# Optimization experiments

Measured on AMD Instinct MI355X. Metric: run time of the kernel, lower is better.

## Reference

```python
import jax, jax.numpy as jnp
import numpy as np

NC = 80
NA = 3
NO = NC + 5  # 85
ANCHORS = jnp.array([[[10.,13.],[16.,30.],[33.,23.]],
                     [[30.,61.],[62.,45.],[59.,119.]],
                     [[116.,90.],[156.,198.],[373.,326.]]], dtype=jnp.float32)
STRIDES = (8.0, 16.0, 32.0)
CONF_THRES = 0.25
IOU_THRES = 0.45
NMS_TOPK = 1000   # fixed candidate count for jit-friendly NMS (YOLO caps at max_nms)
MAX_DET = 300
MAX_WH = 4096.0   # class-offset trick from non_max_suppression


def _decode(x, w, b, anchors, stride):
    # x: [B,C,ny,nx]; w: [255,C]; 1x1 conv == channel matmul
    B, _, ny, nx = x.shape
    y = jnp.einsum('bchw,oc->bohw', x, w) + b[None, :, None, None]
    y = y.reshape(B, NA, NO, ny, nx).transpose(0, 1, 3, 4, 2)  # [B,na,ny,nx,no]
    s = jax.nn.sigmoid(y)
    yv, xv = jnp.meshgrid(jnp.arange(ny, dtype=y.dtype), jnp.arange(nx, dtype=y.dtype), indexing='ij')
    grid = jnp.stack((xv, yv), -1) - 0.5                      # [ny,nx,2]
    xy = (s[..., :2] * 2.0 + grid[None, None]) * stride
    wh = (s[..., 2:4] * 2.0) ** 2 * (anchors * stride)[None, :, None, None, :]
    out = jnp.concatenate((xy, wh, s[..., 4:]), axis=-1)
    return out.reshape(B, NA * ny * nx, NO)


def _xywh2xyxy(x):
    xy, wh = x[..., :2], x[..., 2:4]
    return jnp.concatenate([xy - wh * 0.5, xy + wh * 0.5], axis=-1)


def _box_iou(a, b):
    lt = jnp.maximum(a[:, None, :2], b[None, :, :2])
    rb = jnp.minimum(a[:, None, 2:], b[None, :, 2:])
    wh = jnp.clip(rb - lt, 0.0)
    inter = wh[..., 0] * wh[..., 1]
    area_a = (a[:, 2] - a[:, 0]) * (a[:, 3] - a[:, 1])
    area_b = (b[:, 2] - b[:, 0]) * (b[:, 3] - b[:, 1])
    return inter / (area_a[:, None] + area_b[None, :] - inter + 1e-7)


def _nms_single(pred):
    # pred: [N, 85] -> dets [MAX_DET, 6] = (x1,y1,x2,y2,conf,cls), zero-padded
    boxes = _xywh2xyxy(pred[:, :4])
    obj = pred[:, 4]
    cls_conf = pred[:, 5:] * obj[:, None]          # class scores
    score = jnp.max(cls_conf, axis=-1)
    cls = jnp.argmax(cls_conf, axis=-1)
    score = jnp.where(score > CONF_THRES, score, 0.0)
    top_s, idx = jax.lax.top_k(score, NMS_TOPK)    # fixed candidate set
    b = boxes[idx]                                  # [K,4]
    c = cls[idx].astype(b.dtype)
    bo = b + (c * MAX_WH)[:, None]                  # class-aware offset
    iou = _box_iou(bo, bo)                          # [K,K]
    keep0 = top_s > CONF_THRES
    rng = jnp.arange(NMS_TOPK)

    def body(i, keep):
        sup = (iou[i] > IOU_THRES) & (rng > i)
        return jnp.where(keep[i], keep & (~sup), keep)

    keep = jax.lax.fori_loop(0, NMS_TOPK, body, keep0)
    final_s = jnp.where(keep, top_s, 0.0)
    fs, fi = jax.lax.top_k(final_s, MAX_DET)
    det = jnp.concatenate([b[fi], fs[:, None], c[fi][:, None]], axis=-1)  # [MAX_DET,6]
    det = jnp.where((fs > CONF_THRES)[:, None], det, 0.0)
    return det


def setup_inputs() -> dict:
    key = jax.random.key(0)
    ks = jax.random.split(key, 9)
    B = 16
    return {
        'x0': jax.random.normal(ks[0], (B, 128, 80, 80), jnp.float32),
        'x1': jax.random.normal(ks[1], (B, 256, 40, 40), jnp.float32),
        'x2': jax.random.normal(ks[2], (B, 512, 20, 20), jnp.float32),
        'w0': jax.random.normal(ks[3], (255, 128), jnp.float32) * 0.02,
        'b0': jax.random.normal(ks[4], (255,), jnp.float32) * 0.02,
        'w1': jax.random.normal(ks[5], (255, 256), jnp.float32) * 0.02,
        'b1': jax.random.normal(ks[6], (255,), jnp.float32) * 0.02,
        'w2': jax.random.normal(ks[7], (255, 512), jnp.float32) * 0.02,
        'b2': jax.random.normal(ks[8], (255,), jnp.float32) * 0.02,
    }


def reference(x0, x1, x2, w0, b0, w1, b1, w2, b2):
    z0 = _decode(x0, w0, b0, ANCHORS[0], STRIDES[0])
    z1 = _decode(x1, w1, b1, ANCHORS[1], STRIDES[1])
    z2 = _decode(x2, w2, b2, ANCHORS[2], STRIDES[2])
    pred = jnp.concatenate([z0, z1, z2], axis=1)   # [B, 25200, 85]
    dets = jax.vmap(_nms_single)(pred)             # [B, 300, 6]
    return dets, pred
```

## Files before the change

### kernel.cpp

```cpp
#include <hip/hip_runtime.h>
#include <cstdint>

#define BATCH   16
#define NCLS    80
#define NOUT    85
#define NANC    3
#define NCAND   25200
#define CONF    0.25f
#define IOUT    0.45f
#define TOPK    1000
#define MAXDET  300
#define MAXWH   4096.0f
#define CAPK    2048
#define NBH     520
#define XPAD    40

typedef __attribute__((ext_vector_type(8))) short short8;
typedef __attribute__((ext_vector_type(4))) float f32x4;
typedef unsigned int u32;

constexpr size_t SCORE_OFF = 0;
constexpr size_t CLS_OFF   = SCORE_OFF + (size_t)BATCH * NCAND * 4;
constexpr size_t THR_OFF   = CLS_OFF   + (size_t)BATCH * NCAND * 4;
constexpr size_t CNT_OFF   = THR_OFF   + 256;
constexpr size_t KEYS_OFF  = CNT_OFF   + 256;
constexpr size_t RS_OFF    = KEYS_OFF  + (size_t)BATCH * CAPK * 8;
constexpr size_t RBOX_OFF  = RS_OFF    + (size_t)BATCH * TOPK * 4;
constexpr size_t RBO_OFF   = RBOX_OFF  + (size_t)BATCH * TOPK * 16;
constexpr size_t RCLS_OFF  = RBO_OFF   + (size_t)BATCH * TOPK * 16;
constexpr size_t SUP_OFF   = RCLS_OFF  + (size_t)BATCH * TOPK * 4;
constexpr size_t ORDER_OFF = SUP_OFF   + (size_t)BATCH * TOPK * 16 * 8;
constexpr size_t KC_OFF    = ORDER_OFF + (size_t)BATCH * MAXDET * 4;
constexpr int NL0 = 255 * 128, NL1 = 255 * 256, NL2 = 255 * 512;
constexpr int WB0 = 0, WB1 = 3 * NL0, WB2 = 3 * NL0 + 3 * NL1;

__device__ __forceinline__ ushort bf16rn(float f) {
    uint32_t u = __float_as_uint(f);
    uint32_t r = u + 0x7FFFu + ((u >> 16) & 1u);
    return (ushort)(r >> 16);
}

__device__ __forceinline__ void split3(float v, ushort& s1, ushort& s2, ushort& s3) {
    ushort h1 = bf16rn(v);
    float f1 = __uint_as_float((uint32_t)h1 << 16);
    float r1 = v - f1;
    ushort h2 = bf16rn(r1);
    float f2 = __uint_as_float((uint32_t)h2 << 16);
    ushort h3 = bf16rn(r1 - f2);
    s1 = h1; s2 = h2; s3 = h3;
}

__device__ __forceinline__ void gl_lds16(const float* g, void* l) {
    __builtin_amdgcn_global_load_lds(
        (const __attribute__((address_space(1))) u32*)g,
        (__attribute__((address_space(3))) u32*)l, 16, 0, 0);
}

__global__ __launch_bounds__(256)
void wsplit_kernel(const float* __restrict__ w0, const float* __restrict__ w1,
                   const float* __restrict__ w2, ushort* __restrict__ wsp) {
    int i = blockIdx.x * 256 + threadIdx.x;
    if (i >= NL0 + NL1 + NL2) return;
    const float* src; int idx, base, NL;
    if (i < NL0)            { src = w0; idx = i;             base = WB0; NL = NL0; }
    else if (i < NL0 + NL1) { src = w1; idx = i - NL0;       base = WB1; NL = NL1; }
    else                    { src = w2; idx = i - NL0 - NL1; base = WB2; NL = NL2; }
    ushort s1, s2, s3;
    split3(src[idx], s1, s2, s3);
    wsp[base + idx]          = s1;
    wsp[base + NL + idx]     = s2;
    wsp[base + 2 * NL + idx] = s3;
}

template<int C, int NN>
__device__ __forceinline__ void decode_level(
    const float* __restrict__ xb,
    const ushort* __restrict__ w1p, const ushort* __restrict__ w2p,
    const ushort* __restrict__ w3p, const float* __restrict__ bias,
    float* __restrict__ predB, float* __restrict__ scoreB, int* __restrict__ clsB,
    int tile, int lvlOff, float stride,
    float aw0, float ah0, float aw1, float ah1, float aw2, float ah2,
    char* xsb0, char* xsb1, ushort* x1, ushort* x2, ushort* x3, float* staged)
{
    constexpr int NPOS = NN * NN;
    constexpr int NCHUNK = C / 32;
    constexpr int MAXOFF = C * NPOS - 4;
    const int tid  = threadIdx.x;
    const int lane = tid & 63;
    const int wid  = tid >> 6;
    const int l16  = lane >> 4;
    const int lr   = lane & 15;
    const int pos0 = tile * 64;

    f32x4 acc[4][4];
#pragma unroll
    for (int nf = 0; nf < 4; nf++)
#pragma unroll
        for (int pf = 0; pf < 4; pf++) acc[nf][pf] = (f32x4){0.f, 0.f, 0.f, 0.f};

    const int sp = tid & 63;
    const int wv = tid >> 6;

    char* xsb[2] = {xsb0, xsb1};

#pragma unroll
    for (int i = 0; i < 2; i++) {
        int f = tid + i * 256;
        int kc = f >> 4;
        int p4 = (f & 15) * 4;
        int off = kc * NPOS + pos0 + p4;
        off = off < MAXOFF ? off : MAXOFF;
        gl_lds16(xb + off, xsb[0] + f * 16);
    }

    for (int c = 0; c < NCHUNK; c++) {
        float* xs = (float*)xsb[c & 1];
        __syncthreads();
        if (c + 1 < NCHUNK) {
            const int k0n = (c + 1) * 32;
#pragma unroll
            for (int i = 0; i < 2; i++) {
                int f = tid + i * 256;
                int kc = f >> 4;
                int p4 = (f & 15) * 4;
                int off = (k0n + kc) * NPOS + pos0 + p4;
                off = off < MAXOFF ? off : MAXOFF;
                gl_lds16(xb + off, xsb[(c + 1) & 1] + f * 16);
            }
        }
        {
            short8 s1v, s2v, s3v;
#pragma unroll
            for (int j = 0; j < 8; j++) {
                float f = xs[(wv * 8 + j) * 64 + sp];
                ushort u1, u2, u3;
                split3(f, u1, u2, u3);
                s1v[j] = (short)u1; s2v[j] = (short)u2; s3v[j] = (short)u3;
            }
            int dst = sp * XPAD + ((wv ^ ((sp >> 2) & 3)) << 3);
            *(short8*)(x1 + dst) = s1v;
            *(short8*)(x2 + dst) = s2v;
            *(short8*)(x3 + dst) = s3v;
        }
        asm volatile("s_waitcnt lgkmcnt(0)" ::: "memory");
        __builtin_amdgcn_s_barrier();
        __builtin_amdgcn_sched_barrier(0);
        short8 b1[4], b2[4], b3[4];
#pragma unroll
        for (int pf = 0; pf < 4; pf++) {
            int pr = pf * 16 + lr;
            int off = pr * XPAD + ((l16 ^ (lr >> 2)) << 3);
            b1[pf] = *(const short8*)(x1 + off);
            b2[pf] = *(const short8*)(x2 + off);
            b3[pf] = *(const short8*)(x3 + off);
        }
        const int k0 = c * 32;
#pragma unroll
        for (int nf = 0; nf < 4; nf++) {
            int o = wid * 64 + nf * 16 + lr;
            int oc = o < 255 ? o : 254;
            size_t aoff = (size_t)oc * C + k0 + l16 * 8;
            short8 A1 = *(const short8*)(w1p + aoff);
            short8 A2 = *(const short8*)(w2p + aoff);
            short8 A3 = *(const short8*)(w3p + aoff);
#pragma unroll
            for (int pf = 0; pf < 4; pf++) {
                acc[nf][pf] = __builtin_amdgcn_mfma_f32_16x16x32_bf16(A1, b1[pf], acc[nf][pf], 0, 0, 0);
                acc[nf][pf] = __builtin_amdgcn_mfma_f32_16x16x32_bf16(A1, b2[pf], acc[nf][pf], 0, 0, 0);
                acc[nf][pf] = __builtin_amdgcn_mfma_f32_16x16x32_bf16(A2, b1[pf], acc[nf][pf], 0, 0, 0);
                acc[nf][pf] = __builtin_amdgcn_mfma_f32_16x16x32_bf16(A2, b2[pf], acc[nf][pf], 0, 0, 0);
                acc[nf][pf] = __builtin_amdgcn_mfma_f32_16x16x32_bf16(A1, b3[pf], acc[nf][pf], 0, 0, 0);
                acc[nf][pf] = __builtin_amdgcn_mfma_f32_16x16x32_bf16(A3, b1[pf], acc[nf][pf], 0, 0, 0);
            }
        }
    }

    float bv[16];
#pragma unroll
    for (int nf = 0; nf < 4; nf++)
#pragma unroll
        for (int r = 0; r < 4; r++) {
            int o = wid * 64 + nf * 16 + l16 * 4 + r;
            bv[nf * 4 + r] = (o < 255) ? bias[o] : 0.f;
        }

    const float aw[3] = {aw0, aw1, aw2};
    const float ah[3] = {ah0, ah1, ah2};
    const int validP = (NPOS - pos0) < 64 ? (NPOS - pos0) : 64;

#pragma unroll
    for (int a = 0; a < 3; a++) {
        __syncthreads();
#pragma unroll
        for (int nf = 0; nf < 4; nf++) {
#pragma unroll
            for (int r = 0; r < 4; r++) {
                int o = wid * 64 + nf * 16 + l16 * 4 + r;
                int j = o - a * 85;
                if (o < 255 && j >= 0 && j < 85) {
#pragma unroll
                    for (int pf = 0; pf < 4; pf++) {
                        int p = pf * 16 + lr;
                        int pos = pos0 + p;
                        float y = acc[nf][pf][r] + bv[nf * 4 + r];
                        float s = 1.f / (1.f + __expf(-y));
                        float val;
                        if (j == 0) {
                            int gyi = pos / NN;
                            float gx = (float)(pos - gyi * NN);
                            val = (2.f * s + gx - 0.5f) * stride;
                        } else if (j == 1) {
                            float gy = (float)(pos / NN);
                            val = (2.f * s + gy - 0.5f) * stride;
                        } else if (j == 2) {
                            float t2 = 2.f * s; val = t2 * t2 * aw[a];
                        } else if (j == 3) {
                            float t2 = 2.f * s; val = t2 * t2 * ah[a];
                        } else {
                            val = s;
                        }
                        staged[p * 85 + j] = val;
                    }
                }
            }
        }
        __syncthreads();
        size_t base = ((size_t)lvlOff + (size_t)a * NPOS + pos0) * 85;
        int tot = validP * 85;
        for (int q = tid; q < tot; q += 256)
            predB[base + q] = staged[q];
        int p = tid >> 2, c4 = tid & 3;
        if (p < validP) {
            int j0 = 5 + c4 * 20;
            float best = staged[p * 85 + j0];
            int bi = c4 * 20;
#pragma unroll
            for (int jj = 1; jj < 20; jj++) {
                float vv = staged[p * 85 + j0 + jj];
                if (vv > best) { best = vv; bi = c4 * 20 + jj; }
            }
#pragma unroll
            for (int d = 1; d < 4; d <<= 1) {
                float ov = __shfl_xor(best, d);
                int   oi = __shfl_xor(bi, d);
                if (ov > best || (ov == best && oi < bi)) { best = ov; bi = oi; }
            }
            if (c4 == 0) {
                float obj = staged[p * 85 + 4];
                float sc = obj * best;
                int cand = lvlOff + a * NPOS + pos0 + p;
                scoreB[cand] = (sc > CONF) ? sc : 0.f;
                clsB[cand] = bi;
            }
        }
    }
}

__global__ __launch_bounds__(256)
void decode_all_kernel(const float* __restrict__ x0, const float* __restrict__ x1,
                       const float* __restrict__ x2,
                       const float* __restrict__ b0, const float* __restrict__ b1,
                       const float* __restrict__ b2,
                       const ushort* __restrict__ wsp,
                       float* __restrict__ pred,
                       float* __restrict__ scoreArr, int* __restrict__ clsArr)
{
    __shared__ __align__(16) char smem[31744];
    char*   xsb0 = smem;
    char*   xsb1 = smem + 8192;
    ushort* p1   = (ushort*)(smem + 16384);
    ushort* p2   = (ushort*)(smem + 21504);
    ushort* p3   = (ushort*)(smem + 26624);
    float*  staged = (float*)smem;

    const int b = blockIdx.y;
    const int t = blockIdx.x;

    float* predB  = pred + (size_t)b * NCAND * 85;
    float* scoreB = scoreArr + (size_t)b * NCAND;
    int*   clsB   = clsArr + (size_t)b * NCAND;

    if (t < 7) {
        decode_level<512, 20>(x2 + (size_t)b * 512 * 400,
                              wsp + WB2, wsp + WB2 + NL2, wsp + WB2 + 2 * NL2, b2,
                              predB, scoreB, clsB, t, 24000, 32.f,
                              3712.f, 2880.f, 4992.f, 6336.f, 11936.f, 10432.f,
                              xsb0, xsb1, p1, p2, p3, staged);
    } else if (t < 32) {
        decode_level<256, 40>(x1 + (size_t)b * 256 * 1600,
                              wsp + WB1, wsp + WB1 + NL1, wsp + WB1 + 2 * NL1, b1,
                              predB, scoreB, clsB, t - 7, 19200, 16.f,
                              480.f, 976.f, 992.f, 720.f, 944.f, 1904.f,
                              xsb0, xsb1, p1, p2, p3, staged);
    } else {
        decode_level<128, 80>(x0 + (size_t)b * 128 * 6400,
                              wsp + WB0, wsp + WB0 + NL0, wsp + WB0 + 2 * NL0, b0,
                              predB, scoreB, clsB, t - 32, 0, 8.f,
                              80.f, 104.f, 128.f, 240.f, 264.f, 184.f,
                              xsb0, xsb1, p1, p2, p3, staged);
    }
}

__global__ __launch_bounds__(1024)
void topk_thresh_kernel(const float* __restrict__ score, uint32_t* __restrict__ thrbits,
                        uint32_t* __restrict__ cnt) {
    int img = blockIdx.x, tid = threadIdx.x;
    __shared__ uint32_t h[NBH];
    __shared__ uint32_t sfx[1024 + 1];
    __shared__ int bucketSh;
    for (int i = tid; i < NBH; i += 1024) h[i] = 0;
    __syncthreads();
    const float* s = score + (size_t)img * NCAND;
    for (int i = tid; i < NCAND; i += 1024) {
        float v = s[i];
        if (v > CONF) {
            int bk = (int)((__float_as_uint(v) >> 15) - 0x7D00u);
            bk = bk < 0 ? 0 : (bk >= NBH ? NBH - 1 : bk);
            atomicAdd(&h[bk], 1u);
        }
    }
    __syncthreads();
    sfx[tid] = (tid < NBH) ? h[tid] : 0u;
    if (tid == 0) sfx[1024] = 0u;
    __syncthreads();
    for (int off = 1; off < 1024; off <<= 1) {
        uint32_t v = sfx[tid] + ((tid + off < 1024) ? sfx[tid + off] : 0u);
        __syncthreads();
        sfx[tid] = v;
        __syncthreads();
    }
    uint32_t M = sfx[0];
    uint32_t target = M < TOPK ? M : TOPK;
    if (M > 0 && tid < NBH && sfx[tid] >= target && sfx[tid + 1] < target)
        bucketSh = tid;
    __syncthreads();
    if (tid == 0) {
        thrbits[img] = (M == 0) ? 0xFFFFFFFFu
                                : ((uint32_t)(bucketSh + 0x7D00) << 15);
        cnt[img] = 0u;
    }
}

__global__ __launch_bounds__(256)
void compact_kernel(const float* __restrict__ score, const uint32_t* __restrict__ thrbits,
                    uint32_t* __restrict__ cnt, uint64_t* __restrict__ keys) {
    int img = blockIdx.y;
    int i = blockIdx.x * 256 + threadIdx.x;
    int lane = threadIdx.x & 63;
    uint32_t thr = thrbits[img];
    bool pass = false;
    uint32_t bits = 0;
    if (i < NCAND) {
        float s = score[(size_t)img * NCAND + i];
        bits = __float_as_uint(s);
        pass = (s > CONF) && (bits >= thr);
    }
    unsigned long long m = __ballot(pass);
    if (m) {
        int leader = __ffsll(m) - 1;
        uint32_t base = 0;
        if (lane == leader) base = atomicAdd(&cnt[img], (uint32_t)__popcll(m));
        base = __shfl(base, leader);
        if (pass) {
            uint32_t pos = base + (uint32_t)__popcll(m & ((1ull << lane) - 1ull));
            if (pos < CAPK)
                keys[(size_t)img * CAPK + pos] =
                    ((uint64_t)bits << 32) | (uint32_t)(~(uint32_t)i);
        }
    }
}

__global__ __launch_bounds__(1024)
void sort_kernel(const uint64_t* __restrict__ keys, const uint32_t* __restrict__ cnt,
                 const float* __restrict__ pred, const int* __restrict__ clsArr,
                 float* __restrict__ rs, float* __restrict__ rbox,
                 float* __restrict__ rbo, float* __restrict__ rcls) {
    int img = blockIdx.x, tid = threadIdx.x;
    __shared__ uint64_t sk[CAPK];
    uint32_t n = cnt[img];
    if (n > CAPK) n = CAPK;
    for (int i = tid; i < CAPK; i += 1024)
        sk[i] = (i < (int)n) ? keys[(size_t)img * CAPK + i] : 0ull;
    __syncthreads();
    for (int k = 2; k <= CAPK; k <<= 1)
        for (int j = k >> 1; j > 0; j >>= 1) {
            for (int i = tid; i < CAPK; i += 1024) {
                int l = i ^ j;
                if (l > i) {
                    uint64_t a = sk[i], b = sk[l];
                    bool descRegion = ((i & k) == 0);
                    bool sw = descRegion ? (a < b) : (a > b);
                    if (sw) { sk[i] = b; sk[l] = a; }
                }
            }
            __syncthreads();
        }
    for (int r = tid; r < TOPK; r += 1024) {
        float sc = 0.f; uint32_t idx = 0;
        if (r < (int)n) {
            uint64_t key = sk[r];
            sc = __uint_as_float((uint32_t)(key >> 32));
            idx = ~(uint32_t)key;
        }
        const float* pr = pred + ((size_t)img * NCAND + idx) * 85;
        float cx = pr[0], cy = pr[1], ww = pr[2], hh = pr[3];
        float x1 = cx - ww * 0.5f, y1 = cy - hh * 0.5f;
        float x2 = cx + ww * 0.5f, y2 = cy + hh * 0.5f;
        float c = (float)clsArr[(size_t)img * NCAND + idx];
        float off = c * MAXWH;
        size_t rb = ((size_t)img * TOPK + r) * 4;
        rbox[rb + 0] = x1; rbox[rb + 1] = y1; rbox[rb + 2] = x2; rbox[rb + 3] = y2;
        rbo[rb + 0] = x1 + off; rbo[rb + 1] = y1 + off;
        rbo[rb + 2] = x2 + off; rbo[rb + 3] = y2 + off;
        rs[(size_t)img * TOPK + r] = sc;
        rcls[(size_t)img * TOPK + r] = c;
    }
}

__global__ __launch_bounds__(256)
void sup_kernel(const float* __restrict__ rbo, uint64_t* __restrict__ sup) {
    int img = blockIdx.y;
    int wid = threadIdx.x >> 6, lane = threadIdx.x & 63;
    int i = blockIdx.x * 4 + wid;
    if (i >= TOPK) return;
    const float* bi_ = rbo + ((size_t)img * TOPK + i) * 4;
    float ax1 = bi_[0], ay1 = bi_[1], ax2 = bi_[2], ay2 = bi_[3];
    float areaA = (ax2 - ax1) * (ay2 - ay1);
    for (int w = 0; w < 16; w++) {
        int j = w * 64 + lane;
        bool cond = false;
        if (j < TOPK && j > i) {
            const float* bj = rbo + ((size_t)img * TOPK + j) * 4;
            float bx1 = bj[0], by1 = bj[1], bx2 = bj[2], by2 = bj[3];
            float ltx = fmaxf(ax1, bx1), lty = fmaxf(ay1, by1);
            float rbx = fminf(ax2, bx2), rby = fminf(ay2, by2);
            float iw = fmaxf(rbx - ltx, 0.f), ih = fmaxf(rby - lty, 0.f);
            float inter = iw * ih;
            float areaB = (bx2 - bx1) * (by2 - by1);
            float iou = inter / (areaA + areaB - inter + 1e-7f);
            cond = iou > IOUT;
        }
        unsigned long long m = __ballot(cond);
        if (lane == w) sup[(((size_t)img * TOPK) + i) * 16 + w] = m;
    }
}

__global__ __launch_bounds__(64)
void greedy_kernel(const float* __restrict__ rs, const uint64_t* __restrict__ sup,
                   int* __restrict__ order, int* __restrict__ kcount) {
    int img = blockIdx.x, lane = threadIdx.x;
    __shared__ uint32_t keep32[32];
    __shared__ uint16_t accList[64];
    for (int w = 0; w < 16; w++) {
        int r = w * 64 + lane;
        bool k = (r < TOPK) && (rs[(size_t)img * TOPK + r] > CONF);
        unsigned long long m = __ballot(k);
        if (lane == 0) {
            keep32[2 * w]     = (uint32_t)m;
            keep32[2 * w + 1] = (uint32_t)(m >> 32);
        }
    }
    __syncthreads();
    const uint64_t* supim = sup + (size_t)img * TOPK * 16;
    int kept = 0;
    for (int wb = 0; wb < 16 && kept < MAXDET; wb++) {
        uint64_t word = ((uint64_t)keep32[2 * wb + 1] << 32) | keep32[2 * wb];
        if (!word) continue;
        uint64_t diag = 0;
        int myIdx = wb * 64 + lane;
        if (myIdx < TOPK) diag = supim[(size_t)myIdx * 16 + wb];
        uint64_t cur = word, acc = 0;
        for (int b = 0; b < 64; b++) {
            uint64_t row = __shfl(diag, b);
            if ((cur >> b) & 1ull) { acc |= 1ull << b; cur &= ~row; }
            if (!cur) break;
        }
        int nb = __popcll(acc);
        if (kept + nb > MAXDET) {
            int t = MAXDET - kept;
            bool mine = (acc >> lane) & 1ull;
            int rank = __popcll(acc & ((1ull << lane) - 1ull));
            acc = __ballot(mine && rank < t);
            nb = t;
        }
        {
            bool mine = (acc >> lane) & 1ull;
            int rank = __popcll(acc & ((1ull << lane) - 1ull));
            if (mine) {
                order[img * MAXDET + kept + rank] = wb * 64 + lane;
                accList[rank] = (uint16_t)(wb * 64 + lane);
            }
        }
        kept += nb;
        if (kept >= MAXDET) break;
        __syncthreads();
        int nw = 15 - wb;
        if (nw > 0 && nb > 0) {
            int P = nb * nw;
            for (int p = lane; p < P; p += 64) {
                int bi = p / nw, wq = wb + 1 + p % nw;
                int srcIdx = accList[bi];
                uint64_t row = supim[(size_t)srcIdx * 16 + wq];
                uint32_t lo = (uint32_t)row, hi = (uint32_t)(row >> 32);
                if (lo) atomicAnd(&keep32[2 * wq], ~lo);
                if (hi) atomicAnd(&keep32[2 * wq + 1], ~hi);
            }
        }
        __syncthreads();
    }
    if (lane == 0) kcount[img] = kept;
}

__global__ __launch_bounds__(256)
void final_kernel(const int* __restrict__ order, const int* __restrict__ kcount,
                  const float* __restrict__ rbox, const float* __restrict__ rs,
                  const float* __restrict__ rcls, float* __restrict__ dets) {
    int img = blockIdx.x, tid = threadIdx.x;
    float* d = dets + (size_t)img * MAXDET * 6;
    for (int q = tid; q < MAXDET * 6; q += 256) d[q] = 0.f;
    __syncthreads();
    int kc = kcount[img];
    for (int r = tid; r < kc; r += 256) {
        int i = order[img * MAXDET + r];
        const float* bx = rbox + ((size_t)img * TOPK + i) * 4;
        d[r * 6 + 0] = bx[0]; d[r * 6 + 1] = bx[1];
        d[r * 6 + 2] = bx[2]; d[r * 6 + 3] = bx[3];
        d[r * 6 + 4] = rs[(size_t)img * TOPK + i];
        d[r * 6 + 5] = rcls[(size_t)img * TOPK + i];
    }
}

extern "C" void kernel_launch(void* const* d_in, const int* in_sizes, int n_in,
                              void* d_out, int out_size, void* d_ws, size_t ws_size,
                              hipStream_t stream) {
    const float* x0 = (const float*)d_in[0];
    const float* x1 = (const float*)d_in[1];
    const float* x2 = (const float*)d_in[2];
    const float* w0 = (const float*)d_in[3];
    const float* b0 = (const float*)d_in[4];
    const float* w1 = (const float*)d_in[5];
    const float* b1 = (const float*)d_in[6];
    const float* w2 = (const float*)d_in[7];
    const float* b2 = (const float*)d_in[8];

    float* dets = (float*)d_out;
    float* pred = dets + (size_t)BATCH * MAXDET * 6;

    char* ws = (char*)d_ws;
    float*    scoreArr = (float*)   (ws + SCORE_OFF);
    int*      clsArr   = (int*)     (ws + CLS_OFF);
    uint32_t* thrb     = (uint32_t*)(ws + THR_OFF);
    uint32_t* cnt      = (uint32_t*)(ws + CNT_OFF);
    uint64_t* keys     = (uint64_t*)(ws + KEYS_OFF);
    float*    rs       = (float*)   (ws + RS_OFF);
    float*    rbox     = (float*)   (ws + RBOX_OFF);
    float*    rbo      = (float*)   (ws + RBO_OFF);
    float*    rcls     = (float*)   (ws + RCLS_OFF);
    uint64_t* sup      = (uint64_t*)(ws + SUP_OFF);
    int*      order    = (int*)     (ws + ORDER_OFF);
    int*      kcount   = (int*)     (ws + KC_OFF);
    ushort*   wsp      = (ushort*)  (ws + SUP_OFF);

    wsplit_kernel<<<(NL0 + NL1 + NL2 + 255) / 256, 256, 0, stream>>>(w0, w1, w2, wsp);

    decode_all_kernel<<<dim3(132, BATCH), 256, 0, stream>>>(
        x0, x1, x2, b0, b1, b2, wsp, pred, scoreArr, clsArr);

    topk_thresh_kernel<<<BATCH, 1024, 0, stream>>>(scoreArr, thrb, cnt);
    compact_kernel<<<dim3((NCAND + 255) / 256, BATCH), 256, 0, stream>>>(scoreArr, thrb, cnt, keys);
    sort_kernel<<<BATCH, 1024, 0, stream>>>(keys, cnt, pred, clsArr, rs, rbox, rbo, rcls);
    sup_kernel<<<dim3(250, BATCH), 256, 0, stream>>>(rbo, sup);
    greedy_kernel<<<BATCH, 64, 0, stream>>>(rs, sup, order, kcount);
    final_kernel<<<BATCH, 256, 0, stream>>>(order, kcount, rbox, rs, rcls, dets);
}
```

Before: 309.0 us.

## Halve decode tiles to 32 positions and fuse top-k/NMS tail kernels

Shrinks the decode tile from 64 to 32 spatial positions, doubling the grid and halving LDS per block so more blocks run per CU. It also vectorises the staged pred store and widens the per-position class argmax to 8 lanes. The threshold, compaction and sort kernels are merged into one per-image kernel that compacts candidates into shared memory with LDS atomics. The greedy NMS and final output kernels are merged as well. This removes several launches and global round-trips, at the cost of weight-fragment reuse per block and a serial single-block compaction pass.

Measured after the change: 309.5 us. Within noise of the previous version (+0.2%).

```diff
diff --git a/kernel.cpp b/kernel.cpp
--- a/kernel.cpp
+++ b/kernel.cpp
@@ -29,8 +29,6 @@
 constexpr size_t RBO_OFF   = RBOX_OFF  + (size_t)BATCH * TOPK * 16;
 constexpr size_t RCLS_OFF  = RBO_OFF   + (size_t)BATCH * TOPK * 16;
 constexpr size_t SUP_OFF   = RCLS_OFF  + (size_t)BATCH * TOPK * 4;
-constexpr size_t ORDER_OFF = SUP_OFF   + (size_t)BATCH * TOPK * 16 * 8;
-constexpr size_t KC_OFF    = ORDER_OFF + (size_t)BATCH * MAXDET * 4;
 constexpr int NL0 = 255 * 128, NL1 = 255 * 256, NL2 = 255 * 512;
 constexpr int WB0 = 0, WB1 = 3 * NL0, WB2 = 3 * NL0 + 3 * NL1;
 
@@ -90,27 +88,22 @@
     const int wid  = tid >> 6;
     const int l16  = lane >> 4;
     const int lr   = lane & 15;
-    const int pos0 = tile * 64;
-
-    f32x4 acc[4][4];
+    const int pos0 = tile * 32;
+
+    f32x4 acc[4][2];
 #pragma unroll
     for (int nf = 0; nf < 4; nf++)
 #pragma unroll
-        for (int pf = 0; pf < 4; pf++) acc[nf][pf] = (f32x4){0.f, 0.f, 0.f, 0.f};
-
-    const int sp = tid & 63;
-    const int wv = tid >> 6;
+        for (int pf = 0; pf < 2; pf++) acc[nf][pf] = (f32x4){0.f, 0.f, 0.f, 0.f};
 
     char* xsb[2] = {xsb0, xsb1};
 
-#pragma unroll
-    for (int i = 0; i < 2; i++) {
-        int f = tid + i * 256;
-        int kc = f >> 4;
-        int p4 = (f & 15) * 4;
+    {
+        int kc = tid >> 3;
+        int p4 = (tid & 7) * 4;
         int off = kc * NPOS + pos0 + p4;
         off = off < MAXOFF ? off : MAXOFF;
-        gl_lds16(xb + off, xsb[0] + f * 16);
+        gl_lds16(xb + off, xsb[0] + tid * 16);
     }
 
     for (int c = 0; c < NCHUNK; c++) {
@@ -118,21 +111,19 @@
         __syncthreads();
         if (c + 1 < NCHUNK) {
             const int k0n = (c + 1) * 32;
-#pragma unroll
-            for (int i = 0; i < 2; i++) {
-                int f = tid + i * 256;
-                int kc = f >> 4;
-                int p4 = (f & 15) * 4;
-                int off = (k0n + kc) * NPOS + pos0 + p4;
-                off = off < MAXOFF ? off : MAXOFF;
-                gl_lds16(xb + off, xsb[(c + 1) & 1] + f * 16);
-            }
-        }
-        {
+            int kc = tid >> 3;
+            int p4 = (tid & 7) * 4;
+            int off = (k0n + kc) * NPOS + pos0 + p4;
+            off = off < MAXOFF ? off : MAXOFF;
+            gl_lds16(xb + off, xsb[(c + 1) & 1] + tid * 16);
+        }
+        if (tid < 128) {
+            const int sp = tid & 31;
+            const int wv = tid >> 5;
             short8 s1v, s2v, s3v;
 #pragma unroll
             for (int j = 0; j < 8; j++) {
-                float f = xs[(wv * 8 + j) * 64 + sp];
+                float f = xs[(wv * 8 + j) * 32 + sp];
                 ushort u1, u2, u3;
                 split3(f, u1, u2, u3);
                 s1v[j] = (short)u1; s2v[j] = (short)u2; s3v[j] = (short)u3;
@@ -145,11 +136,11 @@
         asm volatile("s_waitcnt lgkmcnt(0)" ::: "memory");
         __builtin_amdgcn_s_barrier();
         __builtin_amdgcn_sched_barrier(0);
-        short8 b1[4], b2[4], b3[4];
-#pragma unroll
-        for (int pf = 0; pf < 4; pf++) {
+        short8 b1[2], b2[2], b3[2];
+#pragma unroll
+        for (int pf = 0; pf < 2; pf++) {
             int pr = pf * 16 + lr;
-            int off = pr * XPAD + ((l16 ^ (lr >> 2)) << 3);
+            int off = pr * XPAD + ((l16 ^ ((pr >> 2) & 3)) << 3);
             b1[pf] = *(const short8*)(x1 + off);
             b2[pf] = *(const short8*)(x2 + off);
             b3[pf] = *(const short8*)(x3 + off);
@@ -164,7 +155,7 @@
             short8 A2 = *(const short8*)(w2p + aoff);
             short8 A3 = *(const short8*)(w3p + aoff);
 #pragma unroll
-            for (int pf = 0; pf < 4; pf++) {
+            for (int pf = 0; pf < 2; pf++) {
                 acc[nf][pf] = __builtin_amdgcn_mfma_f32_16x16x32_bf16(A1, b1[pf], acc[nf][pf], 0, 0, 0);
                 acc[nf][pf] = __builtin_amdgcn_mfma_f32_16x16x32_bf16(A1, b2[pf], acc[nf][pf], 0, 0, 0);
                 acc[nf][pf] = __builtin_amdgcn_mfma_f32_16x16x32_bf16(A2, b1[pf], acc[nf][pf], 0, 0, 0);
@@ -186,7 +177,7 @@
 
     const float aw[3] = {aw0, aw1, aw2};
     const float ah[3] = {ah0, ah1, ah2};
-    const int validP = (NPOS - pos0) < 64 ? (NPOS - pos0) : 64;
+    const int validP = (NPOS - pos0) < 32 ? (NPOS - pos0) : 32;
 
 #pragma unroll
     for (int a = 0; a < 3; a++) {
@@ -199,7 +190,7 @@
                 int j = o - a * 85;
                 if (o < 255 && j >= 0 && j < 85) {
 #pragma unroll
-                    for (int pf = 0; pf < 4; pf++) {
+                    for (int pf = 0; pf < 2; pf++) {
                         int p = pf * 16 + lr;
                         int pos = pos0 + p;
                         float y = acc[nf][pf][r] + bv[nf * 4 + r];
@@ -226,26 +217,31 @@
         }
         __syncthreads();
         size_t base = ((size_t)lvlOff + (size_t)a * NPOS + pos0) * 85;
-        int tot = validP * 85;
-        for (int q = tid; q < tot; q += 256)
-            predB[base + q] = staged[q];
-        int p = tid >> 2, c4 = tid & 3;
+        if (validP == 32) {
+            const float4* s4 = (const float4*)staged;
+            float4* d4 = (float4*)(predB + base);
+            for (int q = tid; q < (32 * 85 / 4); q += 256) d4[q] = s4[q];
+        } else {
+            int tot = validP * 85;
+            for (int q = tid; q < tot; q += 256) predB[base + q] = staged[q];
+        }
+        int p = tid >> 3, c8 = tid & 7;
         if (p < validP) {
-            int j0 = 5 + c4 * 20;
+            int j0 = 5 + c8 * 10;
             float best = staged[p * 85 + j0];
-            int bi = c4 * 20;
-#pragma unroll
-            for (int jj = 1; jj < 20; jj++) {
+            int bi = c8 * 10;
+#pragma unroll
+            for (int jj = 1; jj < 10; jj++) {
                 float vv = staged[p * 85 + j0 + jj];
-                if (vv > best) { best = vv; bi = c4 * 20 + jj; }
-            }
-#pragma unroll
-            for (int d = 1; d < 4; d <<= 1) {
+                if (vv > best) { best = vv; bi = c8 * 10 + jj; }
+            }
+#pragma unroll
+            for (int d = 1; d < 8; d <<= 1) {
                 float ov = __shfl_xor(best, d);
                 int   oi = __shfl_xor(bi, d);
                 if (ov > best || (ov == best && oi < bi)) { best = ov; bi = oi; }
             }
-            if (c4 == 0) {
+            if (c8 == 0) {
                 float obj = staged[p * 85 + 4];
                 float sc = obj * best;
                 int cand = lvlOff + a * NPOS + pos0 + p;
@@ -265,12 +261,12 @@
                        float* __restrict__ pred,
                        float* __restrict__ scoreArr, int* __restrict__ clsArr)
 {
-    __shared__ __align__(16) char smem[31744];
+    __shared__ __align__(16) char smem[15872];
     char*   xsb0 = smem;
-    char*   xsb1 = smem + 8192;
-    ushort* p1   = (ushort*)(smem + 16384);
-    ushort* p2   = (ushort*)(smem + 21504);
-    ushort* p3   = (ushort*)(smem + 26624);
+    char*   xsb1 = smem + 4096;
+    ushort* p1   = (ushort*)(smem + 8192);
+    ushort* p2   = (ushort*)(smem + 10752);
+    ushort* p3   = (ushort*)(smem + 13312);
     float*  staged = (float*)smem;
 
     const int b = blockIdx.y;
@@ -280,35 +276,41 @@
     float* scoreB = scoreArr + (size_t)b * NCAND;
     int*   clsB   = clsArr + (size_t)b * NCAND;
 
-    if (t < 7) {
+    if (t < 13) {
         decode_level<512, 20>(x2 + (size_t)b * 512 * 400,
                               wsp + WB2, wsp + WB2 + NL2, wsp + WB2 + 2 * NL2, b2,
                               predB, scoreB, clsB, t, 24000, 32.f,
                               3712.f, 2880.f, 4992.f, 6336.f, 11936.f, 10432.f,
                               xsb0, xsb1, p1, p2, p3, staged);
-    } else if (t < 32) {
+    } else if (t < 63) {
         decode_level<256, 40>(x1 + (size_t)b * 256 * 1600,
                               wsp + WB1, wsp + WB1 + NL1, wsp + WB1 + 2 * NL1, b1,
-                              predB, scoreB, clsB, t - 7, 19200, 16.f,
+                              predB, scoreB, clsB, t - 13, 19200, 16.f,
                               480.f, 976.f, 992.f, 720.f, 944.f, 1904.f,
                               xsb0, xsb1, p1, p2, p3, staged);
     } else {
         decode_level<128, 80>(x0 + (size_t)b * 128 * 6400,
                               wsp + WB0, wsp + WB0 + NL0, wsp + WB0 + 2 * NL0, b0,
-                              predB, scoreB, clsB, t - 32, 0, 8.f,
+                              predB, scoreB, clsB, t - 63, 0, 8.f,
                               80.f, 104.f, 128.f, 240.f, 264.f, 184.f,
                               xsb0, xsb1, p1, p2, p3, staged);
     }
 }
 
 __global__ __launch_bounds__(1024)
-void topk_thresh_kernel(const float* __restrict__ score, uint32_t* __restrict__ thrbits,
-                        uint32_t* __restrict__ cnt) {
+void select1_kernel(const float* __restrict__ score, const float* __restrict__ pred,
+                    const int* __restrict__ clsArr, int* __restrict__ nArr,
+                    float* __restrict__ rs, float* __restrict__ rbox,
+                    float* __restrict__ rbo, float* __restrict__ rcls) {
     int img = blockIdx.x, tid = threadIdx.x;
+    __shared__ uint64_t sk[CAPK];
     __shared__ uint32_t h[NBH];
     __shared__ uint32_t sfx[1024 + 1];
     __shared__ int bucketSh;
+    __shared__ uint32_t cntS;
     for (int i = tid; i < NBH; i += 1024) h[i] = 0;
+    for (int i = tid; i < CAPK; i += 1024) sk[i] = 0ull;
+    if (tid == 0) cntS = 0u;
     __syncthreads();
     const float* s = score + (size_t)img * NCAND;
     for (int i = tid; i < NCAND; i += 1024) {
@@ -334,54 +336,20 @@
     if (M > 0 && tid < NBH && sfx[tid] >= target && sfx[tid + 1] < target)
         bucketSh = tid;
     __syncthreads();
-    if (tid == 0) {
-        thrbits[img] = (M == 0) ? 0xFFFFFFFFu
-                                : ((uint32_t)(bucketSh + 0x7D00) << 15);
-        cnt[img] = 0u;
-    }
-}
-
-__global__ __launch_bounds__(256)
-void compact_kernel(const float* __restrict__ score, const uint32_t* __restrict__ thrbits,
-                    uint32_t* __restrict__ cnt, uint64_t* __restrict__ keys) {
-    int img = blockIdx.y;
-    int i = blockIdx.x * 256 + threadIdx.x;
-    int lane = threadIdx.x & 63;
-    uint32_t thr = thrbits[img];
-    bool pass = false;
-    uint32_t bits = 0;
-    if (i < NCAND) {
-        float s = score[(size_t)img * NCAND + i];
-        bits = __float_as_uint(s);
-        pass = (s > CONF) && (bits >= thr);
-    }
-    unsigned long long m = __ballot(pass);
-    if (m) {
-        int leader = __ffsll(m) - 1;
-        uint32_t base = 0;
-        if (lane == leader) base = atomicAdd(&cnt[img], (uint32_t)__popcll(m));
-        base = __shfl(base, leader);
-        if (pass) {
-            uint32_t pos = base + (uint32_t)__popcll(m & ((1ull << lane) - 1ull));
-            if (pos < CAPK)
-                keys[(size_t)img * CAPK + pos] =
-                    ((uint64_t)bits << 32) | (uint32_t)(~(uint32_t)i);
-        }
-    }
-}
-
-__global__ __launch_bounds__(1024)
-void sort_kernel(const uint64_t* __restrict__ keys, const uint32_t* __restrict__ cnt,
-                 const float* __restrict__ pred, const int* __restrict__ clsArr,
-                 float* __restrict__ rs, float* __restrict__ rbox,
-                 float* __restrict__ rbo, float* __restrict__ rcls) {
-    int img = blockIdx.x, tid = threadIdx.x;
-    __shared__ uint64_t sk[CAPK];
-    uint32_t n = cnt[img];
-    if (n > CAPK) n = CAPK;
-    for (int i = tid; i < CAPK; i += 1024)
-        sk[i] = (i < (int)n) ? keys[(size_t)img * CAPK + i] : 0ull;
-    __syncthreads();
+    uint32_t thr = (M == 0) ? 0xFFFFFFFFu : ((uint32_t)(bucketSh + 0x7D00) << 15);
+    for (int i = tid; i < NCAND; i += 1024) {
+        float v = s[i];
+        if (v > CONF) {
+            uint32_t bits = __float_as_uint(v);
+            if (bits >= thr) {
+                uint32_t pos = atomicAdd(&cntS, 1u);
+                if (pos < CAPK)
+                    sk[pos] = ((uint64_t)bits << 32) | (uint32_t)(~(uint32_t)i);
+            }
+        }
+    }
+    __syncthreads();
+    uint32_t n = cntS < CAPK ? cntS : CAPK;
     for (int k = 2; k <= CAPK; k <<= 1)
         for (int j = k >> 1; j > 0; j >>= 1) {
             for (int i = tid; i < CAPK; i += 1024) {
@@ -415,6 +383,7 @@
         rs[(size_t)img * TOPK + r] = sc;
         rcls[(size_t)img * TOPK + r] = c;
     }
+    if (tid == 0) nArr[img] = (int)(n < TOPK ? n : TOPK);
 }
 
 __global__ __launch_bounds__(256)
@@ -446,14 +415,17 @@
 }
 
 __global__ __launch_bounds__(64)
-void greedy_kernel(const float* __restrict__ rs, const uint64_t* __restrict__ sup,
-                   int* __restrict__ order, int* __restrict__ kcount) {
+void greedy_final_kernel(const int* __restrict__ nArr, const uint64_t* __restrict__ sup,
+                         const float* __restrict__ rbox, const float* __restrict__ rs,
+                         const float* __restrict__ rcls, float* __restrict__ dets) {
     int img = blockIdx.x, lane = threadIdx.x;
     __shared__ uint32_t keep32[32];
     __shared__ uint16_t accList[64];
+    __shared__ int ordL[MAXDET];
+    int nkeep = nArr[img];
     for (int w = 0; w < 16; w++) {
         int r = w * 64 + lane;
-        bool k = (r < TOPK) && (rs[(size_t)img * TOPK + r] > CONF);
+        bool k = (r < TOPK) && (r < nkeep);
         unsigned long long m = __ballot(k);
         if (lane == 0) {
             keep32[2 * w]     = (uint32_t)m;
@@ -487,7 +459,7 @@
             bool mine = (acc >> lane) & 1ull;
             int rank = __popcll(acc & ((1ull << lane) - 1ull));
             if (mine) {
-                order[img * MAXDET + kept + rank] = wb * 64 + lane;
+                ordL[kept + rank] = wb * 64 + lane;
                 accList[rank] = (uint16_t)(wb * 64 + lane);
             }
         }
@@ -508,20 +480,12 @@
         }
         __syncthreads();
     }
-    if (lane == 0) kcount[img] = kept;
-}
-
-__global__ __launch_bounds__(256)
-void final_kernel(const int* __restrict__ order, const int* __restrict__ kcount,
-                  const float* __restrict__ rbox, const float* __restrict__ rs,
-                  const float* __restrict__ rcls, float* __restrict__ dets) {
-    int img = blockIdx.x, tid = threadIdx.x;
+    __syncthreads();
     float* d = dets + (size_t)img * MAXDET * 6;
-    for (int q = tid; q < MAXDET * 6; q += 256) d[q] = 0.f;
-    __syncthreads();
-    int kc = kcount[img];
-    for (int r = tid; r < kc; r += 256) {
-        int i = order[img * MAXDET + r];
+    for (int q = lane; q < MAXDET * 6; q += 64) d[q] = 0.f;
+    __syncthreads();
+    for (int r = lane; r < kept; r += 64) {
+        int i = ordL[r];
         const float* bx = rbox + ((size_t)img * TOPK + i) * 4;
         d[r * 6 + 0] = bx[0]; d[r * 6 + 1] = bx[1];
         d[r * 6 + 2] = bx[2]; d[r * 6 + 3] = bx[3];
@@ -549,27 +513,21 @@
     char* ws = (char*)d_ws;
     float*    scoreArr = (float*)   (ws + SCORE_OFF);
     int*      clsArr   = (int*)     (ws + CLS_OFF);
-    uint32_t* thrb     = (uint32_t*)(ws + THR_OFF);
-    uint32_t* cnt      = (uint32_t*)(ws + CNT_OFF);
-    uint64_t* keys     = (uint64_t*)(ws + KEYS_OFF);
+    int*      nArr     = (int*)     (ws + THR_OFF);
     float*    rs       = (float*)   (ws + RS_OFF);
     float*    rbox     = (float*)   (ws + RBOX_OFF);
     float*    rbo      = (float*)   (ws + RBO_OFF);
     float*    rcls     = (float*)   (ws + RCLS_OFF);
     uint64_t* sup      = (uint64_t*)(ws + SUP_OFF);
-    int*      order    = (int*)     (ws + ORDER_OFF);
-    int*      kcount   = (int*)     (ws + KC_OFF);
     ushort*   wsp      = (ushort*)  (ws + SUP_OFF);
 
     wsplit_kernel<<<(NL0 + NL1 + NL2 + 255) / 256, 256, 0, stream>>>(w0, w1, w2, wsp);
 
-    decode_all_kernel<<<dim3(132, BATCH), 256, 0, stream>>>(
+    decode_all_kernel<<<dim3(263, BATCH), 256, 0, stream>>>(
         x0, x1, x2, b0, b1, b2, wsp, pred, scoreArr, clsArr);
 
-    topk_thresh_kernel<<<BATCH, 1024, 0, stream>>>(scoreArr, thrb, cnt);
-    compact_kernel<<<dim3((NCAND + 255) / 256, BATCH), 256, 0, stream>>>(scoreArr, thrb, cnt, keys);
-    sort_kernel<<<BATCH, 1024, 0, stream>>>(keys, cnt, pred, clsArr, rs, rbox, rbo, rcls);
+    select1_kernel<<<BATCH, 1024, 0, stream>>>(scoreArr, pred, clsArr, nArr,
+                                               rs, rbox, rbo, rcls);
     sup_kernel<<<dim3(250, BATCH), 256, 0, stream>>>(rbo, sup);
-    greedy_kernel<<<BATCH, 64, 0, stream>>>(rs, sup, order, kcount);
-    final_kernel<<<BATCH, 256, 0, stream>>>(order, kcount, rbox, rs, rcls, dets);
-}
+    greedy_final_kernel<<<BATCH, 64, 0, stream>>>(nArr, sup, rbox, rs, rcls, dets);
+}
```
